# Optimization experiments

Hardware: AMD Instinct MI355X
Metric: run time of the kernel (lower is better)

The kernel has to match this reference:

```python
import jax, jax.numpy as jnp
import numpy as np

C_IN, C_OUT, K, PAD, STRIDE = 128, 256, 3, 1, 1
H = W = 256


def setup_inputs() -> dict:
    key = jax.random.key(0)
    k1, k2, k3 = jax.random.split(key, 3)
    # batch=1: the original forward uses X_pad[0] for every batch index,
    # so with m=1 the buggy loop and a standard conv are mathematically identical.
    x = jax.random.normal(k1, (1, C_IN, H, W), dtype=jnp.float32)
    # nn.Parameter(torch.rand(...)) -> uniform[0,1)
    weight = jax.random.uniform(k2, (C_OUT, C_IN, K, K), dtype=jnp.float32)
    bias = jax.random.uniform(k3, (C_OUT,), dtype=jnp.float32)
    return {"x": x, "weight": weight, "bias": bias}


def reference(x, weight, bias):
    # Faithful math of convAppx.forward with FP_appx_mul treated as exact
    # multiply (FP_appx_mul is not defined in the source): a plain 2D
    # cross-correlation (no kernel flip, matching the sliced elementwise
    # product) with symmetric padding, stride 1, plus per-channel bias.
    z = jax.lax.conv_general_dilated(
        x, weight,
        window_strides=(STRIDE, STRIDE),
        padding=((PAD, PAD), (PAD, PAD)),
        dimension_numbers=("NCHW", "OIHW", "NCHW"),
    )
    return z + bias[None, :, None, None]
```

## Files before the change

### kernel.cpp

```cpp
#include <hip/hip_runtime.h>
#include <hip/hip_bf16.h>


typedef short bf16x8 __attribute__((ext_vector_type(8)));
typedef float f32x4 __attribute__((ext_vector_type(4)));
typedef unsigned short u16x4 __attribute__((ext_vector_type(4)));
typedef unsigned short u16x8 __attribute__((ext_vector_type(8)));

#define CIN   128
#define COUT  256
#define HH    256
#define WW    256
#define HP    258
#define ROWP  (HP * CIN)

static __device__ __forceinline__ unsigned short f2bf(float v) {
    __hip_bfloat16 b = __float2bfloat16(v);
    return *reinterpret_cast<unsigned short*>(&b);
}

static __device__ __forceinline__ void gload_lds16(const unsigned short* g, unsigned short* l) {
    __builtin_amdgcn_global_load_lds(
        (const __attribute__((address_space(1))) unsigned int*)g,
        (__attribute__((address_space(3))) unsigned int*)l, 16, 0, 0);
}

__global__ __launch_bounds__(256) void xpose_kernel(const float* __restrict__ x,
                                                    unsigned short* __restrict__ xb) {
    int bid = blockIdx.x;
    int h  = bid >> 2;
    int w0 = (bid & 3) * 64;
    __shared__ unsigned short tile[CIN * 72];
    int t = threadIdx.x;

    int wq = t & 15;
    int cib = t >> 4;
    for (int c0 = 0; c0 < CIN; c0 += 16) {
        int ci = c0 + cib;
        float4 v = *(const float4*)(x + ci * (HH * WW) + h * WW + w0 + wq * 4);
        u16x4 p;
        p.x = f2bf(v.x); p.y = f2bf(v.y); p.z = f2bf(v.z); p.w = f2bf(v.w);
        *(u16x4*)(&tile[ci * 72 + wq * 4]) = p;
    }
    __syncthreads();

    for (int it = 0; it < 4; ++it) {
        int idx = it * 256 + t;
        int w  = idx & 63;
        int c8 = idx >> 6;
        u16x8 o;
        #pragma unroll
        for (int j = 0; j < 8; ++j)
            o[j] = tile[(c8 * 8 + j) * 72 + w];
        int dst = ((h + 1) * HP + (w0 + w + 1)) * CIN + c8 * 8;
        *(u16x8*)(&xb[dst]) = o;
    }
}

__global__ __launch_bounds__(256) void zero_edges_kernel(unsigned short* __restrict__ xb) {
    int i = blockIdx.x * 256 + threadIdx.x;
    if (i >= 16448) return;
    u16x8 z = {0, 0, 0, 0, 0, 0, 0, 0};
    int off;
    if (i < 8256) {
        int r   = (i >= 4128) ? 1 : 0;
        int rem = i - r * 4128;
        off = (r * 257) * ROWP + rem * 8;
    } else {
        int j   = i - 8256;
        int col = j >> 12;
        int rem = j & 4095;
        int hp  = (rem >> 4) + 1;
        int c8  = rem & 15;
        off = hp * ROWP + (col * 257) * CIN + c8 * 8;
    }
    *(u16x8*)(&xb[off]) = z;
}

__global__ __launch_bounds__(256) void wreorder_kernel(const float* __restrict__ w,
                                                       unsigned short* __restrict__ wr) {
    int p = blockIdx.x * 256 + threadIdx.x;
    const float* src = w + p * 9;
    #pragma unroll
    for (int khw = 0; khw < 9; ++khw)
        wr[khw * (COUT * CIN) + p] = f2bf(src[khw]);
}

__global__ __launch_bounds__(256) void conv_mfma_kernel(const unsigned short* __restrict__ xb,
                                                        const unsigned short* __restrict__ wr,
                                                        const float* __restrict__ bias,
                                                        float* __restrict__ out) {
    __shared__ unsigned short As[128 * 64];
    __shared__ unsigned short Bs[128 * 64];

    int bid  = blockIdx.x;
    int co_t = bid & 1;
    int wh   = (bid >> 1) & 1;
    int h    = bid >> 2;
    int co0  = co_t * 128;
    int p0   = h * WW + wh * 128;

    int t    = threadIdx.x;
    int wave = t >> 6;
    int lane = t & 63;
    int wm   = wave >> 1;
    int wn   = wave & 1;
    int quad = lane >> 4;
    int l16  = lane & 15;
    int sw   = l16 & 7;

    int lr = lane >> 3;
    int s  = lane & 7;
    int cs = (s ^ lr) * 8;

    f32x4 acc[4][4];
    #pragma unroll
    for (int mi = 0; mi < 4; ++mi)
        #pragma unroll
        for (int ni = 0; ni < 4; ++ni)
            acc[mi][ni] = (f32x4){0.f, 0.f, 0.f, 0.f};

    for (int kh = 0; kh < 3; ++kh) {
        for (int kw = 0; kw < 3; ++kw) {
            int khw = kh * 3 + kw;
            const unsigned short* xsrc = xb + ((h + kh) * HP + wh * 128 + kw) * CIN;
            const unsigned short* wsrc = wr + khw * (COUT * CIN) + co0 * CIN;
            for (int cc = 0; cc < 2; ++cc) {
                int kofs = cc * 64;
                __syncthreads();
                #pragma unroll
                for (int it = 0; it < 4; ++it) {
                    int cid = wave * 4 + it;
                    int r   = cid * 8 + lr;
                    int ge  = kofs + cs;
                    gload_lds16(wsrc + r * CIN + ge, &As[cid * 512]);
                    gload_lds16(xsrc + r * CIN + ge, &Bs[cid * 512]);
                }
                __syncthreads();
                #pragma unroll
                for (int kk = 0; kk < 2; ++kk) {
                    bf16x8 af[4], bfr[4];
                    #pragma unroll
                    for (int mi = 0; mi < 4; ++mi) {
                        int row = wm * 64 + mi * 16 + l16;
                        af[mi] = *(bf16x8*)(&As[row * 64 + ((kk * 4 + quad) ^ sw) * 8]);
                    }
                    #pragma unroll
                    for (int ni = 0; ni < 4; ++ni) {
                        int row = wn * 64 + ni * 16 + l16;
                        bfr[ni] = *(bf16x8*)(&Bs[row * 64 + ((kk * 4 + quad) ^ sw) * 8]);
                    }
                    #pragma unroll
                    for (int mi = 0; mi < 4; ++mi)
                        #pragma unroll
                        for (int ni = 0; ni < 4; ++ni)
                            acc[mi][ni] = __builtin_amdgcn_mfma_f32_16x16x32_bf16(
                                af[mi], bfr[ni], acc[mi][ni], 0, 0, 0);
                }
            }
        }
    }

    #pragma unroll
    for (int mi = 0; mi < 4; ++mi) {
        #pragma unroll
        for (int r = 0; r < 4; ++r) {
            int co = co0 + wm * 64 + mi * 16 + quad * 4 + r;
            float b = bias[co];
            float* orow = out + co * (HH * WW) + p0 + wn * 64 + l16;
            #pragma unroll
            for (int ni = 0; ni < 4; ++ni)
                orow[ni * 16] = acc[mi][ni][r] + b;
        }
    }
}

extern "C" void kernel_launch(void* const* d_in, const int* in_sizes, int n_in,
                              void* d_out, int out_size, void* d_ws, size_t ws_size,
                              hipStream_t stream) {
    const float* x    = (const float*)d_in[0];
    const float* w    = (const float*)d_in[1];
    const float* bias = (const float*)d_in[2];
    float* out        = (float*)d_out;

    unsigned short* xb = (unsigned short*)d_ws;
    unsigned short* wr = xb + (size_t)HP * HP * CIN;

    xpose_kernel<<<dim3(1024), dim3(256), 0, stream>>>(x, xb);
    zero_edges_kernel<<<dim3(65), dim3(256), 0, stream>>>(xb);
    wreorder_kernel<<<dim3(128), dim3(256), 0, stream>>>(w, wr);
    conv_mfma_kernel<<<dim3(1024), dim3(256), 0, stream>>>(xb, wr, bias, out);
}
```

Baseline: 143.4 us.

## Load weight fragments directly from global memory and fold edge zeroing into transpose

The conv kernel stops staging weights through LDS. Each lane now loads its A-operand bf16x8 fragments straight from global memory into registers before the barrier, which halves LDS use and the async LDS copies per step. The zero-padding kernel is merged into the first 65 blocks of the transpose kernel to save a launch, and the kh/kw/cc loops are fully unrolled. The cost is more global/L2 traffic, since each wave reads its own weight rows without sharing them through LDS, more register pressure, and possible global-load latency stalls before the MFMAs.

```diff
diff --git a/kernel.cpp b/kernel.cpp
--- a/kernel.cpp
+++ b/kernel.cpp
@@ -33,6 +33,27 @@
     __shared__ unsigned short tile[CIN * 72];
     int t = threadIdx.x;
 
+    if (bid < 65) {
+        int i = bid * 256 + t;
+        if (i < 16448) {
+            u16x8 z = {0, 0, 0, 0, 0, 0, 0, 0};
+            int off;
+            if (i < 8256) {
+                int r   = (i >= 4128) ? 1 : 0;
+                int rem = i - r * 4128;
+                off = (r * 257) * ROWP + rem * 8;
+            } else {
+                int j   = i - 8256;
+                int col = j >> 12;
+                int rem = j & 4095;
+                int hp  = (rem >> 4) + 1;
+                int c8  = rem & 15;
+                off = hp * ROWP + (col * 257) * CIN + c8 * 8;
+            }
+            *(u16x8*)(&xb[off]) = z;
+        }
+    }
+
     int wq = t & 15;
     int cib = t >> 4;
     for (int c0 = 0; c0 < CIN; c0 += 16) {
@@ -57,26 +78,6 @@
     }
 }
 
-__global__ __launch_bounds__(256) void zero_edges_kernel(unsigned short* __restrict__ xb) {
-    int i = blockIdx.x * 256 + threadIdx.x;
-    if (i >= 16448) return;
-    u16x8 z = {0, 0, 0, 0, 0, 0, 0, 0};
-    int off;
-    if (i < 8256) {
-        int r   = (i >= 4128) ? 1 : 0;
-        int rem = i - r * 4128;
-        off = (r * 257) * ROWP + rem * 8;
-    } else {
-        int j   = i - 8256;
-        int col = j >> 12;
-        int rem = j & 4095;
-        int hp  = (rem >> 4) + 1;
-        int c8  = rem & 15;
-        off = hp * ROWP + (col * 257) * CIN + c8 * 8;
-    }
-    *(u16x8*)(&xb[off]) = z;
-}
-
 __global__ __launch_bounds__(256) void wreorder_kernel(const float* __restrict__ w,
                                                        unsigned short* __restrict__ wr) {
     int p = blockIdx.x * 256 + threadIdx.x;
@@ -90,7 +91,6 @@
                                                         const unsigned short* __restrict__ wr,
                                                         const float* __restrict__ bias,
                                                         float* __restrict__ out) {
-    __shared__ unsigned short As[128 * 64];
     __shared__ unsigned short Bs[128 * 64];
 
     int bid  = blockIdx.x;
@@ -113,6 +113,8 @@
     int s  = lane & 7;
     int cs = (s ^ lr) * 8;
 
+    const unsigned short* abase = wr + (size_t)(co0 + wm * 64 + l16) * CIN;
+
     f32x4 acc[4][4];
     #pragma unroll
     for (int mi = 0; mi < 4; ++mi)
@@ -120,31 +122,33 @@
         for (int ni = 0; ni < 4; ++ni)
             acc[mi][ni] = (f32x4){0.f, 0.f, 0.f, 0.f};
 
+    #pragma unroll
     for (int kh = 0; kh < 3; ++kh) {
+        #pragma unroll
         for (int kw = 0; kw < 3; ++kw) {
             int khw = kh * 3 + kw;
             const unsigned short* xsrc = xb + ((h + kh) * HP + wh * 128 + kw) * CIN;
-            const unsigned short* wsrc = wr + khw * (COUT * CIN) + co0 * CIN;
+            const unsigned short* asrc = abase + (size_t)khw * (COUT * CIN);
+            #pragma unroll
             for (int cc = 0; cc < 2; ++cc) {
                 int kofs = cc * 64;
+                bf16x8 af[2][4];
+                #pragma unroll
+                for (int kk = 0; kk < 2; ++kk)
+                    #pragma unroll
+                    for (int mi = 0; mi < 4; ++mi)
+                        af[kk][mi] = *(const bf16x8*)(asrc + mi * 16 * CIN + kofs + kk * 32 + quad * 8);
                 __syncthreads();
                 #pragma unroll
                 for (int it = 0; it < 4; ++it) {
                     int cid = wave * 4 + it;
                     int r   = cid * 8 + lr;
-                    int ge  = kofs + cs;
-                    gload_lds16(wsrc + r * CIN + ge, &As[cid * 512]);
-                    gload_lds16(xsrc + r * CIN + ge, &Bs[cid * 512]);
+                    gload_lds16(xsrc + r * CIN + kofs + cs, &Bs[cid * 512]);
                 }
                 __syncthreads();
                 #pragma unroll
                 for (int kk = 0; kk < 2; ++kk) {
-                    bf16x8 af[4], bfr[4];
-                    #pragma unroll
-                    for (int mi = 0; mi < 4; ++mi) {
-                        int row = wm * 64 + mi * 16 + l16;
-                        af[mi] = *(bf16x8*)(&As[row * 64 + ((kk * 4 + quad) ^ sw) * 8]);
-                    }
+                    bf16x8 bfr[4];
                     #pragma unroll
                     for (int ni = 0; ni < 4; ++ni) {
                         int row = wn * 64 + ni * 16 + l16;
@@ -155,7 +159,7 @@
                         #pragma unroll
                         for (int ni = 0; ni < 4; ++ni)
                             acc[mi][ni] = __builtin_amdgcn_mfma_f32_16x16x32_bf16(
-                                af[mi], bfr[ni], acc[mi][ni], 0, 0, 0);
+                                af[kk][mi], bfr[ni], acc[mi][ni], 0, 0, 0);
                 }
             }
         }
@@ -187,7 +191,6 @@
     unsigned short* wr = xb + (size_t)HP * HP * CIN;
 
     xpose_kernel<<<dim3(1024), dim3(256), 0, stream>>>(x, xb);
-    zero_edges_kernel<<<dim3(65), dim3(256), 0, stream>>>(xb);
     wreorder_kernel<<<dim3(128), dim3(256), 0, stream>>>(w, wr);
     conv_mfma_kernel<<<dim3(1024), dim3(256), 0, stream>>>(xb, wr, bias, out);
 }
```

Result: slower. 175.2 us (+22.1%).
